# Kernel tuning notes

Hardware: AMD Instinct MI355X
Metric: run time of the kernel (lower is better)

## Reference

```python
import jax, jax.numpy as jnp
import numpy as np
import math

B, S, D = 2, 2048, 512
H = 8
DEPTH = D // H
MAX_REL = 1024
NEG_INF = -1.0e9


def skew(t):
    # t: (..., r, c). Pad a zero column on the left, reshape to move relative
    # logits into their absolute positions (Music Transformer skew trick).
    r, c = t.shape[-2], t.shape[-1]
    padded = jnp.pad(t, [(0, 0)] * (t.ndim - 1) + [(1, 0)])
    s = padded.reshape(-1, c + 1, r)[:, 1:]
    return s.reshape(t.shape)


def setup_inputs() -> dict:
    key = jax.random.key(0)
    ks = jax.random.split(key, 12)
    sc = 1.0 / math.sqrt(D)
    return {
        "q": jax.random.normal(ks[0], (B, S, D), jnp.float32),
        "k": jax.random.normal(ks[1], (B, S, D), jnp.float32),
        "v": jax.random.normal(ks[2], (B, S, D), jnp.float32),
        "mask": jax.random.randint(ks[3], (B, 1, S, S), 0, 2, jnp.int32),
        "Wq_w": jax.random.normal(ks[4], (D, D), jnp.float32) * sc,
        "Wq_b": jnp.zeros((D,), jnp.float32),
        "Wk_w": jax.random.normal(ks[5], (D, D), jnp.float32) * sc,
        "Wk_b": jnp.zeros((D,), jnp.float32),
        "Wv_w": jax.random.normal(ks[6], (D, D), jnp.float32) * sc,
        "Wv_b": jnp.zeros((D,), jnp.float32),
        "E": jax.random.normal(ks[7], (MAX_REL, D), jnp.float32),
        "Wo_w": jax.random.normal(ks[8], (D, D), jnp.float32) * sc,
        "Wo_b": jnp.zeros((D,), jnp.float32),
    }


def reference(q, k, v, mask, Wq_w, Wq_b, Wk_w, Wk_b, Wv_w, Wv_b, E, Wo_w, Wo_b):
    # Linear projections (torch Linear: x @ W^T + b)
    qp = q @ Wq_w.T + Wq_b
    kp = k @ Wk_w.T + Wk_b
    vp = v @ Wv_w.T + Wv_b

    # Required relative position embeddings for seq_len S (S >= MAX_REL here:
    # repeat E[0] for the first S-MAX_REL positions, then the full table).
    n_rep = max(0, S - MAX_REL)
    e = jnp.concatenate([jnp.tile(E[0:1], (n_rep, 1)), E[max(0, MAX_REL - S):]], axis=0)  # (S, D)

    # Split heads: (B,S,D)->(B,H,S,depth); e: (S,D)->(H,S,depth)
    qh = qp.reshape(B, S, H, DEPTH).transpose(0, 2, 1, 3)
    kh = kp.reshape(B, S, H, DEPTH).transpose(0, 2, 1, 3)
    vh = vp.reshape(B, S, H, DEPTH).transpose(0, 2, 1, 3)
    eh = e.reshape(S, H, DEPTH).transpose(1, 0, 2)

    QKt = jnp.einsum('bhqd,bhkd->bhqk', qh, kh)
    Srel = skew(jnp.einsum('bhqd,hkd->bhqk', qh, eh))
    logits = (QKt + Srel) / math.sqrt(DEPTH)
    logits = logits + mask.astype(logits.dtype) * NEG_INF
    attn = jnp.einsum('bhqk,bhkd->bhqd', jax.nn.softmax(logits, axis=-1), vh)

    # Merge heads and output projection
    out = attn.transpose(0, 2, 1, 3).reshape(B, S, D)
    return out @ Wo_w.T + Wo_b
```

## Files before the change

### kernel.cpp

```cpp
#include <hip/hip_runtime.h>
#include <hip/hip_bf16.h>

#define BB 2
#define SS 2048
#define DD 512
#define HH 8
#define DP 64
#define MR 1024

typedef __attribute__((ext_vector_type(8))) short bf16x8;
typedef __attribute__((ext_vector_type(4))) float floatx4;

static __device__ __forceinline__ unsigned short f2b(float x) {
    __hip_bfloat16 h = __float2bfloat16(x);
    return *reinterpret_cast<unsigned short*>(&h);
}
static __device__ __forceinline__ float b2f(unsigned short u) {
    __hip_bfloat16 h = *reinterpret_cast<__hip_bfloat16*>(&u);
    return __bfloat162float(h);
}
static __device__ __forceinline__ void gll16(const void* g, void* l) {
    __builtin_amdgcn_global_load_lds(
        (const __attribute__((address_space(1))) void*)g,
        (__attribute__((address_space(3))) void*)l, 16, 0, 0);
}
static __device__ __forceinline__ int xoff(int ks, int quad, int row) {
    return (((ks * 4 + quad) ^ (row & 7)) * 16);
}

__global__ __launch_bounds__(256) void prep_kernel(
    const float* __restrict__ Wq, const float* __restrict__ Wk,
    const float* __restrict__ Wv, const float* __restrict__ Wo,
    const float* __restrict__ E,  const float* __restrict__ q,
    const float* __restrict__ k,  const float* __restrict__ v,
    const int* __restrict__ mask,
    unsigned short* __restrict__ Wqb, unsigned short* __restrict__ Wkb,
    unsigned short* __restrict__ Wvb, unsigned short* __restrict__ Wob,
    unsigned short* __restrict__ Eb,  unsigned short* __restrict__ qb16,
    unsigned short* __restrict__ kb16, unsigned short* __restrict__ vb16,
    unsigned long long* __restrict__ bits)
{
    const int blk = blockIdx.x;
    if (blk < 7680) {
        const int gid = blk * 256 + threadIdx.x;
        const float* src; unsigned short* dst; int off;
        if      (gid < 65536)   { src = Wq; dst = Wqb;  off = gid; }
        else if (gid < 131072)  { src = Wk; dst = Wkb;  off = gid - 65536; }
        else if (gid < 196608)  { src = Wv; dst = Wvb;  off = gid - 131072; }
        else if (gid < 262144)  { src = Wo; dst = Wob;  off = gid - 196608; }
        else if (gid < 393216)  { src = E;  dst = Eb;   off = gid - 262144; }
        else if (gid < 917504)  { src = q;  dst = qb16; off = gid - 393216; }
        else if (gid < 1441792) { src = k;  dst = kb16; off = gid - 917504; }
        else                    { src = v;  dst = vb16; off = gid - 1441792; }
        float4 x = ((const float4*)src)[off];
        ushort4 u; u.x = f2b(x.x); u.y = f2b(x.y); u.z = f2b(x.z); u.w = f2b(x.w);
        ((ushort4*)dst)[off] = u;
    } else {
        const size_t wid = (size_t)(blk - 7680) * 4 + (threadIdx.x >> 6);
        const int lane = threadIdx.x & 63;
        const int mv = mask[wid * 64 + lane];
        unsigned long long bal = __ballot(mv != 0);
        if (lane == 0) bits[wid] = bal;
    }
}

__global__ __launch_bounds__(256) void gemm_proj(
    const unsigned short* __restrict__ Xq, const unsigned short* __restrict__ Xk,
    const unsigned short* __restrict__ Xv,
    const unsigned short* __restrict__ Wqb, const unsigned short* __restrict__ Wkb,
    const unsigned short* __restrict__ Wvb,
    const float* __restrict__ bq, const float* __restrict__ bk,
    const float* __restrict__ bv,
    unsigned short* __restrict__ qp, unsigned short* __restrict__ kp,
    unsigned short* __restrict__ vpT)
{
    const int z = blockIdx.z;
    const unsigned short* A  = (z == 0) ? Xq : (z == 1) ? Xk : Xv;
    const unsigned short* Wb = (z == 0) ? Wqb : (z == 1) ? Wkb : Wvb;
    const float* bias        = (z == 0) ? bq : (z == 1) ? bk : bv;

    __shared__ __align__(16) char parena[16384];
    char* AsB = parena;
    char* WsB = parena + 8192;
    const int t = threadIdx.x, lane = t & 63, w = t >> 6;
    const int quad = lane >> 4, l15 = lane & 15;
    const int wm = w >> 1, wn = w & 1;
    const int m0 = blockIdx.x * 64, n0 = blockIdx.y * 64;

    int wrow[2], wcol[2];
#pragma unroll
    for (int i = 0; i < 2; i++) {
        const int c = w * 128 + i * 64 + lane;
        wrow[i] = c >> 3; wcol[i] = (c & 7) ^ (wrow[i] & 7);
    }

    floatx4 acc[2][2];
#pragma unroll
    for (int i = 0; i < 2; i++)
#pragma unroll
        for (int j = 0; j < 2; j++) acc[i][j] = (floatx4){0.f, 0.f, 0.f, 0.f};

    for (int k0 = 0; k0 < 512; k0 += 64) {
        if (k0) __syncthreads();
#pragma unroll
        for (int i = 0; i < 2; i++) {
            gll16(A  + (size_t)(m0 + wrow[i]) * 512 + k0 + wcol[i] * 8,
                  AsB + (w * 2 + i) * 1024);
            gll16(Wb + (size_t)(n0 + wrow[i]) * 512 + k0 + wcol[i] * 8,
                  WsB + (w * 2 + i) * 1024);
        }
        __syncthreads();
#pragma unroll
        for (int ks = 0; ks < 2; ks++) {
            bf16x8 a0 = *(const bf16x8*)(AsB + (wm * 32 + l15) * 128 + xoff(ks, quad, l15));
            bf16x8 a1 = *(const bf16x8*)(AsB + (wm * 32 + 16 + l15) * 128 + xoff(ks, quad, l15));
            bf16x8 b0 = *(const bf16x8*)(WsB + (wn * 32 + l15) * 128 + xoff(ks, quad, l15));
            bf16x8 b1 = *(const bf16x8*)(WsB + (wn * 32 + 16 + l15) * 128 + xoff(ks, quad, l15));
            acc[0][0] = __builtin_amdgcn_mfma_f32_16x16x32_bf16(a0, b0, acc[0][0], 0, 0, 0);
            acc[0][1] = __builtin_amdgcn_mfma_f32_16x16x32_bf16(a0, b1, acc[0][1], 0, 0, 0);
            acc[1][0] = __builtin_amdgcn_mfma_f32_16x16x32_bf16(a1, b0, acc[1][0], 0, 0, 0);
            acc[1][1] = __builtin_amdgcn_mfma_f32_16x16x32_bf16(a1, b1, acc[1][1], 0, 0, 0);
        }
    }

    if (z < 2) {
        unsigned short* Out = (z == 0) ? qp : kp;
#pragma unroll
        for (int sub = 0; sub < 2; sub++)
#pragma unroll
            for (int ct = 0; ct < 2; ct++) {
                const int n = n0 + wn * 32 + ct * 16 + l15;
                const float bvl = bias[n];
#pragma unroll
                for (int r = 0; r < 4; r++) {
                    const size_t m = (size_t)(m0 + wm * 32 + sub * 16 + quad * 4 + r);
                    Out[m * 512 + n] = f2b(acc[sub][ct][r] + bvl);
                }
            }
    } else {
        __syncthreads();
        unsigned short* Ls = (unsigned short*)parena;
#pragma unroll
        for (int sub = 0; sub < 2; sub++)
#pragma unroll
            for (int ct = 0; ct < 2; ct++) {
                const int dcol = wn * 32 + ct * 16 + l15;
                const float bvl = bias[n0 + dcol];
#pragma unroll
                for (int r = 0; r < 4; r++) {
                    const int scol = wm * 32 + sub * 16 + quad * 4 + r;
                    Ls[dcol * 72 + scol] = f2b(acc[sub][ct][r] + bvl);
                }
            }
        __syncthreads();
        const int bb = blockIdx.x >> 5, s0 = (blockIdx.x & 31) * 64, hh = blockIdx.y;
#pragma unroll
        for (int p = 0; p < 2; p++) {
            const int idx = p * 256 + t;
            const int row = idx >> 3, c8 = (idx & 7) * 8;
            *(uint4*)&vpT[((size_t)(bb * 8 + hh) * 64 + row) * SS + s0 + c8] =
                *(const uint4*)&Ls[row * 72 + c8];
        }
    }
}

__global__ __launch_bounds__(256) void gemm_out(
    const unsigned short* __restrict__ A, const unsigned short* __restrict__ Wb,
    const float* __restrict__ bias, float* __restrict__ Out)
{
    __shared__ __align__(16) char parena[16384];
    char* AsB = parena;
    char* WsB = parena + 8192;
    const int t = threadIdx.x, lane = t & 63, w = t >> 6;
    const int quad = lane >> 4, l15 = lane & 15;
    const int wm = w >> 1, wn = w & 1;
    const int m0 = blockIdx.x * 64, n0 = blockIdx.y * 64;

    int wrow[2], wcol[2];
#pragma unroll
    for (int i = 0; i < 2; i++) {
        const int c = w * 128 + i * 64 + lane;
        wrow[i] = c >> 3; wcol[i] = (c & 7) ^ (wrow[i] & 7);
    }

    floatx4 acc[2][2];
#pragma unroll
    for (int i = 0; i < 2; i++)
#pragma unroll
        for (int j = 0; j < 2; j++) acc[i][j] = (floatx4){0.f, 0.f, 0.f, 0.f};

    for (int k0 = 0; k0 < 512; k0 += 64) {
        if (k0) __syncthreads();
#pragma unroll
        for (int i = 0; i < 2; i++) {
            gll16(A  + (size_t)(m0 + wrow[i]) * 512 + k0 + wcol[i] * 8,
                  AsB + (w * 2 + i) * 1024);
            gll16(Wb + (size_t)(n0 + wrow[i]) * 512 + k0 + wcol[i] * 8,
                  WsB + (w * 2 + i) * 1024);
        }
        __syncthreads();
#pragma unroll
        for (int ks = 0; ks < 2; ks++) {
            bf16x8 a0 = *(const bf16x8*)(AsB + (wm * 32 + l15) * 128 + xoff(ks, quad, l15));
            bf16x8 a1 = *(const bf16x8*)(AsB + (wm * 32 + 16 + l15) * 128 + xoff(ks, quad, l15));
            bf16x8 b0 = *(const bf16x8*)(WsB + (wn * 32 + l15) * 128 + xoff(ks, quad, l15));
            bf16x8 b1 = *(const bf16x8*)(WsB + (wn * 32 + 16 + l15) * 128 + xoff(ks, quad, l15));
            acc[0][0] = __builtin_amdgcn_mfma_f32_16x16x32_bf16(a0, b0, acc[0][0], 0, 0, 0);
            acc[0][1] = __builtin_amdgcn_mfma_f32_16x16x32_bf16(a0, b1, acc[0][1], 0, 0, 0);
            acc[1][0] = __builtin_amdgcn_mfma_f32_16x16x32_bf16(a1, b0, acc[1][0], 0, 0, 0);
            acc[1][1] = __builtin_amdgcn_mfma_f32_16x16x32_bf16(a1, b1, acc[1][1], 0, 0, 0);
        }
    }
#pragma unroll
    for (int sub = 0; sub < 2; sub++)
#pragma unroll
        for (int ct = 0; ct < 2; ct++) {
            const int n = n0 + wn * 32 + ct * 16 + l15;
            const float bvl = bias[n];
#pragma unroll
            for (int r = 0; r < 4; r++) {
                const size_t m = (size_t)(m0 + wm * 32 + sub * 16 + quad * 4 + r);
                Out[m * 512 + n] = acc[sub][ct][r] + bvl;
            }
        }
}

__global__ __launch_bounds__(256) void relg_kernel(
    const unsigned short* __restrict__ qp, const unsigned short* __restrict__ Eb,
    unsigned short* __restrict__ G)
{
    __shared__ unsigned short Ls[64 * 72];
    const int t = threadIdx.x, lane = t & 63, w = t >> 6;
    const int quad = lane >> 4, l15 = lane & 15;
    const int bh = blockIdx.z, b = bh >> 3, h = bh & 7;
    const int i0b = blockIdx.x * 64, t0 = blockIdx.y * 64;

    const unsigned short* Ar = qp + ((size_t)b * SS + i0b + w * 16 + l15) * DD + h * DP;
    bf16x8 a0 = *(const bf16x8*)(Ar + quad * 8);
    bf16x8 a1 = *(const bf16x8*)(Ar + 32 + quad * 8);

    floatx4 acc[4];
#pragma unroll
    for (int ct = 0; ct < 4; ct++) acc[ct] = (floatx4){0.f, 0.f, 0.f, 0.f};
#pragma unroll
    for (int ct = 0; ct < 4; ct++) {
        const unsigned short* Br = Eb + (size_t)(t0 + ct * 16 + l15) * DD + h * DP;
        bf16x8 b0 = *(const bf16x8*)(Br + quad * 8);
        bf16x8 b1 = *(const bf16x8*)(Br + 32 + quad * 8);
        acc[ct] = __builtin_amdgcn_mfma_f32_16x16x32_bf16(a0, b0, acc[ct], 0, 0, 0);
        acc[ct] = __builtin_amdgcn_mfma_f32_16x16x32_bf16(a1, b1, acc[ct], 0, 0, 0);
    }
#pragma unroll
    for (int ct = 0; ct < 4; ct++)
#pragma unroll
        for (int r = 0; r < 4; r++)
            Ls[(w * 16 + quad * 4 + r) * 72 + ct * 16 + l15] = f2b(acc[ct][r]);
    __syncthreads();
#pragma unroll
    for (int p = 0; p < 2; p++) {
        const int idx = p * 256 + t;
        const int row = idx >> 3, c8 = (idx & 7) * 8;
        *(uint4*)&G[((size_t)bh * SS + i0b + row) * MR + t0 + c8] =
            *(const uint4*)&Ls[row * 72 + c8];
    }
}

__global__ __launch_bounds__(256, 4) void attn_kernel(
    const unsigned short* __restrict__ qp, const unsigned short* __restrict__ kp,
    const unsigned short* __restrict__ vpT, const unsigned long long* __restrict__ mb64,
    const unsigned short* __restrict__ G, unsigned short* __restrict__ ao)
{
    __shared__ __align__(16) char smem[33024];
    char* KsB = smem;
    char* VtB = smem + 16384;

    const int t = threadIdx.x, lane = t & 63, w = t >> 6;
    const int quad = lane >> 4, l15 = lane & 15;
    const int wr = w >> 1, kh = w & 1;
    const int bh = blockIdx.y, b = bh >> 3, h = bh & 7;
    const int i0w = blockIdx.x * 32 + wr * 16;
    const int gi = i0w + l15;

    const unsigned short* kb = kp + (size_t)b * SS * DD + h * DP;
    const unsigned short* vb = vpT + (size_t)bh * DP * SS;
    const unsigned short* Gb = G + (size_t)bh * SS * MR;
    const unsigned long long* mrow64 = mb64 + ((size_t)b * SS + gi) * 32;

    const unsigned short* qrow = qp + ((size_t)b * SS + gi) * DD + h * DP;
    bf16x8 qf0 = *(const bf16x8*)(qrow + quad * 8);
    bf16x8 qf1 = *(const bf16x8*)(qrow + 32 + quad * 8);

    const unsigned short* pdiag = Gb + (size_t)gi * 1023;
    const float d0a = b2f(Gb[(size_t)gi * MR]);
    const float d0b = b2f(Gb[(size_t)min(gi + 1, SS - 1) * MR]);

    char* KhB = KsB + kh * 8192;
    char* VhB = VtB + kh * 8192;
    char* PtB = KhB + wr * 4096;

    int koff[4], voff[4];
#pragma unroll
    for (int i = 0; i < 4; i++) {
        const int c = wr * 256 + i * 64 + lane;
        const int crow = c >> 3, ccol = (c & 7) ^ (crow & 7);
        koff[i] = crow * DD + ccol * 8;
        voff[i] = crow * SS + ccol * 8;
    }

    floatx4 oacc[4];
#pragma unroll
    for (int ct = 0; ct < 4; ct++) oacc[ct] = (floatx4){0.f, 0.f, 0.f, 0.f};
    float lsum = 0.0f;

    for (int it = 0; it < 16; it++) {
        const int k0 = (kh * 16 + it) * 64;
        __syncthreads();
#pragma unroll
        for (int i = 0; i < 4; i++)
            gll16(kb + (size_t)k0 * DD + koff[i], KhB + (wr * 4 + i) * 1024);
#pragma unroll
        for (int i = 0; i < 4; i++)
            gll16(vb + k0 + voff[i], VhB + (wr * 4 + i) * 1024);

        const unsigned long long mwv = mrow64[kh * 16 + it];
        const unsigned int mlo = (unsigned int)mwv;
        const unsigned int mhi = (unsigned int)(mwv >> 32);

        float relv[4][4];
#pragma unroll
        for (int ct = 0; ct < 4; ct++) {
            const int k0c = k0 + ct * 16;
            const int gj0 = k0c + quad * 4;
            const int dmax = i0w + 15 - k0c;
            const int dmin = i0w - (k0c + 15);
            if (dmin >= MR) {
#pragma unroll
                for (int r = 0; r < 4; r++) relv[ct][r] = d0a;
            } else if (dmin >= 0 && dmax <= MR - 1) {
#pragma unroll
                for (int r = 0; r < 4; r++) relv[ct][r] = b2f(pdiag[1023 + gj0 + r]);
            } else if (dmax <= -2 && dmin >= -(MR + 1)) {
#pragma unroll
                for (int r = 0; r < 4; r++) relv[ct][r] = d0b;
            } else if (dmax <= -(MR + 2)) {
#pragma unroll
                for (int r = 0; r < 4; r++) relv[ct][r] = b2f(pdiag[gj0 - 2 + r]);
            } else {
#pragma unroll
                for (int r = 0; r < 4; r++) {
                    const int gj = gj0 + r;
                    const int dd = gi - gj;
                    float rl;
                    if (dd >= MR) rl = d0a;
                    else if (dd >= 0) rl = b2f(pdiag[1023 + gj]);
                    else if (dd == -1) rl = 0.0f;
                    else if (dd >= -(MR + 1)) rl = d0b;
                    else rl = b2f(pdiag[gj - 2]);
                    relv[ct][r] = rl;
                }
            }
        }
        __syncthreads();

        ushort4 pu[4];
#pragma unroll
        for (int ct = 0; ct < 4; ct++) {
            const unsigned int half = (ct < 2) ? mlo : mhi;
            const unsigned int nib = (half >> ((ct & 1) * 16 + quad * 4)) & 0xFu;
            floatx4 acc;
#pragma unroll
            for (int r = 0; r < 4; r++)
                acc[r] = relv[ct][r] + (((nib >> r) & 1u) ? -8.0e9f : 0.0f);
            const int row = ct * 16 + l15;
            bf16x8 kf0 = *(const bf16x8*)(KhB + row * 128 + xoff(0, quad, l15));
            bf16x8 kf1 = *(const bf16x8*)(KhB + row * 128 + xoff(1, quad, l15));
            acc = __builtin_amdgcn_mfma_f32_16x16x32_bf16(kf0, qf0, acc, 0, 0, 0);
            acc = __builtin_amdgcn_mfma_f32_16x16x32_bf16(kf1, qf1, acc, 0, 0, 0);
            const float p0 = __expf(acc[0] * 0.125f - 18.75f);
            const float p1 = __expf(acc[1] * 0.125f - 18.75f);
            const float p2 = __expf(acc[2] * 0.125f - 18.75f);
            const float p3 = __expf(acc[3] * 0.125f - 18.75f);
            lsum += (p0 + p1) + (p2 + p3);
            pu[ct].x = f2b(p0); pu[ct].y = f2b(p1);
            pu[ct].z = f2b(p2); pu[ct].w = f2b(p3);
        }
        __syncthreads();

#pragma unroll
        for (int ct = 0; ct < 4; ct++)
            *(ushort4*)(PtB + l15 * 144 + ct * 32 + quad * 8) = pu[ct];

        bf16x8 pt0 = *(const bf16x8*)(PtB + l15 * 144 + quad * 16);
        bf16x8 pt1 = *(const bf16x8*)(PtB + l15 * 144 + 64 + quad * 16);
#pragma unroll
        for (int ct = 0; ct < 4; ct++) {
            const int drow = ct * 16 + l15;
            bf16x8 vf0 = *(const bf16x8*)(VhB + drow * 128 + xoff(0, quad, l15));
            bf16x8 vf1 = *(const bf16x8*)(VhB + drow * 128 + xoff(1, quad, l15));
            oacc[ct] = __builtin_amdgcn_mfma_f32_16x16x32_bf16(vf0, pt0, oacc[ct], 0, 0, 0);
            oacc[ct] = __builtin_amdgcn_mfma_f32_16x16x32_bf16(vf1, pt1, oacc[ct], 0, 0, 0);
        }
    }

    lsum += __shfl_xor(lsum, 16);
    lsum += __shfl_xor(lsum, 32);

    __syncthreads();
    float* OmW = (float*)(VtB + wr * 4352);
    float* MlW = (float*)(smem + 32768);
    if (kh == 1) {
#pragma unroll
        for (int ct = 0; ct < 4; ct++)
            *(floatx4*)&OmW[l15 * 68 + ct * 16 + quad * 4] = oacc[ct];
        if (lane < 16) MlW[wr * 16 + lane] = lsum;
    }
    __syncthreads();
    if (kh == 0) {
        const float inv = 1.0f / (lsum + MlW[wr * 16 + l15]);
#pragma unroll
        for (int ct = 0; ct < 4; ct++) {
            floatx4 o1 = *(const floatx4*)&OmW[l15 * 68 + ct * 16 + quad * 4];
            ushort4 u;
            u.x = f2b((oacc[ct][0] + o1[0]) * inv);
            u.y = f2b((oacc[ct][1] + o1[1]) * inv);
            u.z = f2b((oacc[ct][2] + o1[2]) * inv);
            u.w = f2b((oacc[ct][3] + o1[3]) * inv);
            *(ushort4*)&ao[((size_t)b * SS + gi) * DD + h * DP + ct * 16 + quad * 4] = u;
        }
    }
}

extern "C" void kernel_launch(void* const* d_in, const int* in_sizes, int n_in,
                              void* d_out, int out_size, void* d_ws, size_t ws_size,
                              hipStream_t stream)
{
    const float* q    = (const float*)d_in[0];
    const float* k    = (const float*)d_in[1];
    const float* v    = (const float*)d_in[2];
    const int*   mask = (const int*)d_in[3];
    const float* Wq_w = (const float*)d_in[4];
    const float* Wq_b = (const float*)d_in[5];
    const float* Wk_w = (const float*)d_in[6];
    const float* Wk_b = (const float*)d_in[7];
    const float* Wv_w = (const float*)d_in[8];
    const float* Wv_b = (const float*)d_in[9];
    const float* E    = (const float*)d_in[10];
    const float* Wo_w = (const float*)d_in[11];
    const float* Wo_b = (const float*)d_in[12];
    float* out = (float*)d_out;

    char* ws = (char*)d_ws;
    unsigned short* G    = (unsigned short*)ws;
    unsigned short* qp   = (unsigned short*)(ws + 67108864);
    unsigned short* kp   = qp + 2097152;
    unsigned short* vpT  = kp + 2 * 2097152;
    unsigned short* qb16 = vpT + 2097152;
    unsigned short* kb16 = qb16 + 2097152;
    unsigned short* vb16 = kb16 + 2097152;
    unsigned short* aob  = qb16;
    unsigned long long* mbits = (unsigned long long*)(ws + 67108864 + 7 * 4194304);
    unsigned short* Wqb = (unsigned short*)(ws + 67108864 + 7 * 4194304 + 1048576);
    unsigned short* Wkb = Wqb + 262144;
    unsigned short* Wvb = Wkb + 262144;
    unsigned short* Wob = Wvb + 262144;
    unsigned short* Ebf = Wob + 262144;

    dim3 blk(256);
    hipLaunchKernelGGL(prep_kernel, dim3(40448), blk, 0, stream,
                       Wq_w, Wk_w, Wv_w, Wo_w, E, q, k, v, mask,
                       Wqb, Wkb, Wvb, Wob, Ebf, qb16, kb16, vb16, mbits);
    hipLaunchKernelGGL(gemm_proj, dim3(64, 8, 3), blk, 0, stream,
                       qb16, kb16, vb16, Wqb, Wkb, Wvb, Wq_b, Wk_b, Wv_b,
                       qp, kp, vpT);
    hipLaunchKernelGGL(relg_kernel, dim3(32, 16, 16), blk, 0, stream, qp, Ebf, G);
    hipLaunchKernelGGL(attn_kernel, dim3(64, 16), blk, 0, stream,
                       qp, kp, vpT, mbits, G, aob);
    hipLaunchKernelGGL(gemm_out, dim3(64, 8), blk, 0, stream, aob, Wob, Wo_b, out);
}
```

Measured before the change: 266.1 us.

## Double-buffer attention K/V tiles with prefetch, halve GEMM M-tiles

The attention kernel now processes 32-key tiles and double-buffers K and V in shared memory. The next tile's global-to-LDS loads are issued before computing the current one, and the mask word and relative-position values for the next tile are loaded early, which removes one barrier per iteration. The projection and output GEMMs use 32-row M tiles, doubling the grid for more parallelism at the cost of less reuse per block. It also adds smaller MFMA chunks per iteration and more loop iterations.

```diff
diff --git a/kernel.cpp b/kernel.cpp
--- a/kernel.cpp
+++ b/kernel.cpp
@@ -79,88 +79,76 @@
     const unsigned short* Wb = (z == 0) ? Wqb : (z == 1) ? Wkb : Wvb;
     const float* bias        = (z == 0) ? bq : (z == 1) ? bk : bv;
 
-    __shared__ __align__(16) char parena[16384];
+    __shared__ __align__(16) char parena[12288];
     char* AsB = parena;
-    char* WsB = parena + 8192;
+    char* WsB = parena + 4096;
     const int t = threadIdx.x, lane = t & 63, w = t >> 6;
     const int quad = lane >> 4, l15 = lane & 15;
     const int wm = w >> 1, wn = w & 1;
-    const int m0 = blockIdx.x * 64, n0 = blockIdx.y * 64;
-
+    const int m0 = blockIdx.x * 32, n0 = blockIdx.y * 64;
+
+    const int pa = w * 64 + lane;
+    const int arow = pa >> 3, acol = (pa & 7) ^ (arow & 7);
     int wrow[2], wcol[2];
 #pragma unroll
     for (int i = 0; i < 2; i++) {
-        const int c = w * 128 + i * 64 + lane;
-        wrow[i] = c >> 3; wcol[i] = (c & 7) ^ (wrow[i] & 7);
-    }
-
-    floatx4 acc[2][2];
-#pragma unroll
-    for (int i = 0; i < 2; i++)
-#pragma unroll
-        for (int j = 0; j < 2; j++) acc[i][j] = (floatx4){0.f, 0.f, 0.f, 0.f};
+        const int c = w * 2 + i;
+        const int p = c * 64 + lane;
+        wrow[i] = p >> 3; wcol[i] = (p & 7) ^ (wrow[i] & 7);
+    }
+
+    floatx4 acc[2];
+    acc[0] = (floatx4){0.f, 0.f, 0.f, 0.f};
+    acc[1] = (floatx4){0.f, 0.f, 0.f, 0.f};
 
     for (int k0 = 0; k0 < 512; k0 += 64) {
         if (k0) __syncthreads();
-#pragma unroll
-        for (int i = 0; i < 2; i++) {
-            gll16(A  + (size_t)(m0 + wrow[i]) * 512 + k0 + wcol[i] * 8,
-                  AsB + (w * 2 + i) * 1024);
+        gll16(A + (size_t)(m0 + arow) * 512 + k0 + acol * 8, AsB + w * 1024);
+#pragma unroll
+        for (int i = 0; i < 2; i++)
             gll16(Wb + (size_t)(n0 + wrow[i]) * 512 + k0 + wcol[i] * 8,
                   WsB + (w * 2 + i) * 1024);
-        }
         __syncthreads();
 #pragma unroll
         for (int ks = 0; ks < 2; ks++) {
-            bf16x8 a0 = *(const bf16x8*)(AsB + (wm * 32 + l15) * 128 + xoff(ks, quad, l15));
-            bf16x8 a1 = *(const bf16x8*)(AsB + (wm * 32 + 16 + l15) * 128 + xoff(ks, quad, l15));
+            bf16x8 a0 = *(const bf16x8*)(AsB + (wm * 16 + l15) * 128 + xoff(ks, quad, l15));
             bf16x8 b0 = *(const bf16x8*)(WsB + (wn * 32 + l15) * 128 + xoff(ks, quad, l15));
             bf16x8 b1 = *(const bf16x8*)(WsB + (wn * 32 + 16 + l15) * 128 + xoff(ks, quad, l15));
-            acc[0][0] = __builtin_amdgcn_mfma_f32_16x16x32_bf16(a0, b0, acc[0][0], 0, 0, 0);
-            acc[0][1] = __builtin_amdgcn_mfma_f32_16x16x32_bf16(a0, b1, acc[0][1], 0, 0, 0);
-            acc[1][0] = __builtin_amdgcn_mfma_f32_16x16x32_bf16(a1, b0, acc[1][0], 0, 0, 0);
-            acc[1][1] = __builtin_amdgcn_mfma_f32_16x16x32_bf16(a1, b1, acc[1][1], 0, 0, 0);
+            acc[0] = __builtin_amdgcn_mfma_f32_16x16x32_bf16(a0, b0, acc[0], 0, 0, 0);
+            acc[1] = __builtin_amdgcn_mfma_f32_16x16x32_bf16(a0, b1, acc[1], 0, 0, 0);
         }
     }
 
     if (z < 2) {
         unsigned short* Out = (z == 0) ? qp : kp;
 #pragma unroll
-        for (int sub = 0; sub < 2; sub++)
-#pragma unroll
-            for (int ct = 0; ct < 2; ct++) {
-                const int n = n0 + wn * 32 + ct * 16 + l15;
-                const float bvl = bias[n];
-#pragma unroll
-                for (int r = 0; r < 4; r++) {
-                    const size_t m = (size_t)(m0 + wm * 32 + sub * 16 + quad * 4 + r);
-                    Out[m * 512 + n] = f2b(acc[sub][ct][r] + bvl);
-                }
+        for (int ct = 0; ct < 2; ct++) {
+            const int n = n0 + wn * 32 + ct * 16 + l15;
+            const float bvl = bias[n];
+#pragma unroll
+            for (int r = 0; r < 4; r++) {
+                const size_t m = (size_t)(m0 + wm * 16 + quad * 4 + r);
+                Out[m * 512 + n] = f2b(acc[ct][r] + bvl);
             }
+        }
     } else {
         __syncthreads();
         unsigned short* Ls = (unsigned short*)parena;
 #pragma unroll
-        for (int sub = 0; sub < 2; sub++)
-#pragma unroll
-            for (int ct = 0; ct < 2; ct++) {
-                const int dcol = wn * 32 + ct * 16 + l15;
-                const float bvl = bias[n0 + dcol];
-#pragma unroll
-                for (int r = 0; r < 4; r++) {
-                    const int scol = wm * 32 + sub * 16 + quad * 4 + r;
-                    Ls[dcol * 72 + scol] = f2b(acc[sub][ct][r] + bvl);
-                }
+        for (int ct = 0; ct < 2; ct++) {
+            const int dcol = wn * 32 + ct * 16 + l15;
+            const float bvl = bias[n0 + dcol];
+#pragma unroll
+            for (int r = 0; r < 4; r++) {
+                const int srow = wm * 16 + quad * 4 + r;
+                Ls[dcol * 40 + srow] = f2b(acc[ct][r] + bvl);
             }
+        }
         __syncthreads();
-        const int bb = blockIdx.x >> 5, s0 = (blockIdx.x & 31) * 64, hh = blockIdx.y;
-#pragma unroll
-        for (int p = 0; p < 2; p++) {
-            const int idx = p * 256 + t;
-            const int row = idx >> 3, c8 = (idx & 7) * 8;
-            *(uint4*)&vpT[((size_t)(bb * 8 + hh) * 64 + row) * SS + s0 + c8] =
-                *(const uint4*)&Ls[row * 72 + c8];
-        }
+        const int bb = blockIdx.x >> 6, s0 = (blockIdx.x & 63) * 32, hh = blockIdx.y;
+        const int drow = t >> 2, sc8 = (t & 3) * 8;
+        *(uint4*)&vpT[((size_t)(bb * 8 + hh) * 64 + drow) * SS + s0 + sc8] =
+            *(const uint4*)&Ls[drow * 40 + sc8];
     }
 }
 
@@ -168,61 +156,55 @@
     const unsigned short* __restrict__ A, const unsigned short* __restrict__ Wb,
     const float* __restrict__ bias, float* __restrict__ Out)
 {
-    __shared__ __align__(16) char parena[16384];
+    __shared__ __align__(16) char parena[12288];
     char* AsB = parena;
-    char* WsB = parena + 8192;
+    char* WsB = parena + 4096;
     const int t = threadIdx.x, lane = t & 63, w = t >> 6;
     const int quad = lane >> 4, l15 = lane & 15;
     const int wm = w >> 1, wn = w & 1;
-    const int m0 = blockIdx.x * 64, n0 = blockIdx.y * 64;
-
+    const int m0 = blockIdx.x * 32, n0 = blockIdx.y * 64;
+
+    const int pa = w * 64 + lane;
+    const int arow = pa >> 3, acol = (pa & 7) ^ (arow & 7);
     int wrow[2], wcol[2];
 #pragma unroll
     for (int i = 0; i < 2; i++) {
-        const int c = w * 128 + i * 64 + lane;
-        wrow[i] = c >> 3; wcol[i] = (c & 7) ^ (wrow[i] & 7);
-    }
-
-    floatx4 acc[2][2];
-#pragma unroll
-    for (int i = 0; i < 2; i++)
-#pragma unroll
-        for (int j = 0; j < 2; j++) acc[i][j] = (floatx4){0.f, 0.f, 0.f, 0.f};
+        const int c = w * 2 + i;
+        const int p = c * 64 + lane;
+        wrow[i] = p >> 3; wcol[i] = (p & 7) ^ (wrow[i] & 7);
+    }
+
+    floatx4 acc[2];
+    acc[0] = (floatx4){0.f, 0.f, 0.f, 0.f};
+    acc[1] = (floatx4){0.f, 0.f, 0.f, 0.f};
 
     for (int k0 = 0; k0 < 512; k0 += 64) {
         if (k0) __syncthreads();
-#pragma unroll
-        for (int i = 0; i < 2; i++) {
-            gll16(A  + (size_t)(m0 + wrow[i]) * 512 + k0 + wcol[i] * 8,
-                  AsB + (w * 2 + i) * 1024);
+        gll16(A + (size_t)(m0 + arow) * 512 + k0 + acol * 8, AsB + w * 1024);
+#pragma unroll
+        for (int i = 0; i < 2; i++)
             gll16(Wb + (size_t)(n0 + wrow[i]) * 512 + k0 + wcol[i] * 8,
                   WsB + (w * 2 + i) * 1024);
-        }
         __syncthreads();
 #pragma unroll
         for (int ks = 0; ks < 2; ks++) {
-            bf16x8 a0 = *(const bf16x8*)(AsB + (wm * 32 + l15) * 128 + xoff(ks, quad, l15));
-            bf16x8 a1 = *(const bf16x8*)(AsB + (wm * 32 + 16 + l15) * 128 + xoff(ks, quad, l15));
+            bf16x8 a0 = *(const bf16x8*)(AsB + (wm * 16 + l15) * 128 + xoff(ks, quad, l15));
             bf16x8 b0 = *(const bf16x8*)(WsB + (wn * 32 + l15) * 128 + xoff(ks, quad, l15));
             bf16x8 b1 = *(const bf16x8*)(WsB + (wn * 32 + 16 + l15) * 128 + xoff(ks, quad, l15));
-            acc[0][0] = __builtin_amdgcn_mfma_f32_16x16x32_bf16(a0, b0, acc[0][0], 0, 0, 0);
-            acc[0][1] = __builtin_amdgcn_mfma_f32_16x16x32_bf16(a0, b1, acc[0][1], 0, 0, 0);
-            acc[1][0] = __builtin_amdgcn_mfma_f32_16x16x32_bf16(a1, b0, acc[1][0], 0, 0, 0);
-            acc[1][1] = __builtin_amdgcn_mfma_f32_16x16x32_bf16(a1, b1, acc[1][1], 0, 0, 0);
-        }
-    }
-#pragma unroll
-    for (int sub = 0; sub < 2; sub++)
-#pragma unroll
-        for (int ct = 0; ct < 2; ct++) {
-            const int n = n0 + wn * 32 + ct * 16 + l15;
-            const float bvl = bias[n];
-#pragma unroll
-            for (int r = 0; r < 4; r++) {
-                const size_t m = (size_t)(m0 + wm * 32 + sub * 16 + quad * 4 + r);
-                Out[m * 512 + n] = acc[sub][ct][r] + bvl;
-            }
-        }
+            acc[0] = __builtin_amdgcn_mfma_f32_16x16x32_bf16(a0, b0, acc[0], 0, 0, 0);
+            acc[1] = __builtin_amdgcn_mfma_f32_16x16x32_bf16(a0, b1, acc[1], 0, 0, 0);
+        }
+    }
+#pragma unroll
+    for (int ct = 0; ct < 2; ct++) {
+        const int n = n0 + wn * 32 + ct * 16 + l15;
+        const float bvl = bias[n];
+#pragma unroll
+        for (int r = 0; r < 4; r++) {
+            const size_t m = (size_t)(m0 + wm * 16 + quad * 4 + r);
+            Out[m * 512 + n] = acc[ct][r] + bvl;
+        }
+    }
 }
 
 __global__ __launch_bounds__(256) void relg_kernel(
@@ -265,15 +247,51 @@
     }
 }
 
+static __device__ __forceinline__ void load_rel(
+    const unsigned short* __restrict__ pdiag, int i0w, int gi, int k0,
+    float d0a, float d0b, int quad, float relv[2][4])
+{
+#pragma unroll
+    for (int ct = 0; ct < 2; ct++) {
+        const int k0c = k0 + ct * 16;
+        const int gj0 = k0c + quad * 4;
+        const int dmax = i0w + 15 - k0c;
+        const int dmin = i0w - (k0c + 15);
+        if (dmin >= MR) {
+#pragma unroll
+            for (int r = 0; r < 4; r++) relv[ct][r] = d0a;
+        } else if (dmin >= 0 && dmax <= MR - 1) {
+#pragma unroll
+            for (int r = 0; r < 4; r++) relv[ct][r] = b2f(pdiag[1023 + gj0 + r]);
+        } else if (dmax <= -2 && dmin >= -(MR + 1)) {
+#pragma unroll
+            for (int r = 0; r < 4; r++) relv[ct][r] = d0b;
+        } else if (dmax <= -(MR + 2)) {
+#pragma unroll
+            for (int r = 0; r < 4; r++) relv[ct][r] = b2f(pdiag[gj0 - 2 + r]);
+        } else {
+#pragma unroll
+            for (int r = 0; r < 4; r++) {
+                const int gj = gj0 + r;
+                const int dd = gi - gj;
+                float rl;
+                if (dd >= MR) rl = d0a;
+                else if (dd >= 0) rl = b2f(pdiag[1023 + gj]);
+                else if (dd == -1) rl = 0.0f;
+                else if (dd >= -(MR + 1)) rl = d0b;
+                else rl = b2f(pdiag[gj - 2]);
+                relv[ct][r] = rl;
+            }
+        }
+    }
+}
+
 __global__ __launch_bounds__(256, 4) void attn_kernel(
     const unsigned short* __restrict__ qp, const unsigned short* __restrict__ kp,
-    const unsigned short* __restrict__ vpT, const unsigned long long* __restrict__ mb64,
+    const unsigned short* __restrict__ vpT, const unsigned int* __restrict__ mb32,
     const unsigned short* __restrict__ G, unsigned short* __restrict__ ao)
 {
-    __shared__ __align__(16) char smem[33024];
-    char* KsB = smem;
-    char* VtB = smem + 16384;
-
+    __shared__ __align__(16) char smem[38016];
     const int t = threadIdx.x, lane = t & 63, w = t >> 6;
     const int quad = lane >> 4, l15 = lane & 15;
     const int wr = w >> 1, kh = w & 1;
@@ -284,7 +302,7 @@
     const unsigned short* kb = kp + (size_t)b * SS * DD + h * DP;
     const unsigned short* vb = vpT + (size_t)bh * DP * SS;
     const unsigned short* Gb = G + (size_t)bh * SS * MR;
-    const unsigned long long* mrow64 = mb64 + ((size_t)b * SS + gi) * 32;
+    const unsigned int* mrow32 = mb32 + ((size_t)b * SS + gi) * 64;
 
     const unsigned short* qrow = qp + ((size_t)b * SS + gi) * DD + h * DP;
     bf16x8 qf0 = *(const bf16x8*)(qrow + quad * 8);
@@ -294,17 +312,20 @@
     const float d0a = b2f(Gb[(size_t)gi * MR]);
     const float d0b = b2f(Gb[(size_t)min(gi + 1, SS - 1) * MR]);
 
-    char* KhB = KsB + kh * 8192;
-    char* VhB = VtB + kh * 8192;
-    char* PtB = KhB + wr * 4096;
-
-    int koff[4], voff[4];
-#pragma unroll
-    for (int i = 0; i < 4; i++) {
-        const int c = wr * 256 + i * 64 + lane;
-        const int crow = c >> 3, ccol = (c & 7) ^ (crow & 7);
-        koff[i] = crow * DD + ccol * 8;
-        voff[i] = crow * SS + ccol * 8;
+    char* Kh = smem + kh * 8192;
+    char* Vh = smem + 16384 + kh * 8192;
+    char* Pt = smem + 32768 + w * 1280;
+
+    int kofs[2], vofs[2], dst[2];
+#pragma unroll
+    for (int i = 0; i < 2; i++) {
+        const int c = wr * 2 + i;
+        const int p = c * 64 + lane;
+        const int krow = p >> 3, kcol = (p & 7) ^ (krow & 7);
+        kofs[i] = krow * DD + kcol * 8;
+        const int vrow = p >> 2, vcol = (p & 3) ^ (vrow & 3);
+        vofs[i] = vrow * SS + vcol * 8;
+        dst[i] = c * 1024;
     }
 
     floatx4 oacc[4];
@@ -312,93 +333,78 @@
     for (int ct = 0; ct < 4; ct++) oacc[ct] = (floatx4){0.f, 0.f, 0.f, 0.f};
     float lsum = 0.0f;
 
-    for (int it = 0; it < 16; it++) {
-        const int k0 = (kh * 16 + it) * 64;
+    {
+        const int k0 = kh * 1024;
+        gll16(kb + (size_t)k0 * DD + kofs[0], Kh + dst[0]);
+        gll16(kb + (size_t)k0 * DD + kofs[1], Kh + dst[1]);
+        gll16(vb + k0 + vofs[0], Vh + dst[0]);
+        gll16(vb + k0 + vofs[1], Vh + dst[1]);
+    }
+    unsigned int mwv = mrow32[kh * 32];
+    float relv[2][4];
+    load_rel(pdiag, i0w, gi, kh * 1024, d0a, d0b, quad, relv);
+
+    for (int it = 0; it < 32; it++) {
+        const int cur = it & 1;
         __syncthreads();
-#pragma unroll
-        for (int i = 0; i < 4; i++)
-            gll16(kb + (size_t)k0 * DD + koff[i], KhB + (wr * 4 + i) * 1024);
-#pragma unroll
-        for (int i = 0; i < 4; i++)
-            gll16(vb + k0 + voff[i], VhB + (wr * 4 + i) * 1024);
-
-        const unsigned long long mwv = mrow64[kh * 16 + it];
-        const unsigned int mlo = (unsigned int)mwv;
-        const unsigned int mhi = (unsigned int)(mwv >> 32);
-
-        float relv[4][4];
-#pragma unroll
-        for (int ct = 0; ct < 4; ct++) {
-            const int k0c = k0 + ct * 16;
-            const int gj0 = k0c + quad * 4;
-            const int dmax = i0w + 15 - k0c;
-            const int dmin = i0w - (k0c + 15);
-            if (dmin >= MR) {
-#pragma unroll
-                for (int r = 0; r < 4; r++) relv[ct][r] = d0a;
-            } else if (dmin >= 0 && dmax <= MR - 1) {
-#pragma unroll
-                for (int r = 0; r < 4; r++) relv[ct][r] = b2f(pdiag[1023 + gj0 + r]);
-            } else if (dmax <= -2 && dmin >= -(MR + 1)) {
-#pragma unroll
-                for (int r = 0; r < 4; r++) relv[ct][r] = d0b;
-            } else if (dmax <= -(MR + 2)) {
-#pragma unroll
-                for (int r = 0; r < 4; r++) relv[ct][r] = b2f(pdiag[gj0 - 2 + r]);
-            } else {
-#pragma unroll
-                for (int r = 0; r < 4; r++) {
-                    const int gj = gj0 + r;
-                    const int dd = gi - gj;
-                    float rl;
-                    if (dd >= MR) rl = d0a;
-                    else if (dd >= 0) rl = b2f(pdiag[1023 + gj]);
-                    else if (dd == -1) rl = 0.0f;
-                    else if (dd >= -(MR + 1)) rl = d0b;
-                    else rl = b2f(pdiag[gj - 2]);
-                    relv[ct][r] = rl;
-                }
-            }
-        }
-        __syncthreads();
-
-        ushort4 pu[4];
-#pragma unroll
-        for (int ct = 0; ct < 4; ct++) {
-            const unsigned int half = (ct < 2) ? mlo : mhi;
-            const unsigned int nib = (half >> ((ct & 1) * 16 + quad * 4)) & 0xFu;
-            floatx4 acc;
+        if (it + 1 < 32) {
+            const int k0n = kh * 1024 + (it + 1) * 32;
+            const int nb = (cur ^ 1) * 4096;
+            gll16(kb + (size_t)k0n * DD + kofs[0], Kh + nb + dst[0]);
+            gll16(kb + (size_t)k0n * DD + kofs[1], Kh + nb + dst[1]);
+            gll16(vb + k0n + vofs[0], Vh + nb + dst[0]);
+            gll16(vb + k0n + vofs[1], Vh + nb + dst[1]);
+        }
+        const unsigned int mcur = mwv;
+        float relc[2][4];
+#pragma unroll
+        for (int ct = 0; ct < 2; ct++)
+#pragma unroll
+            for (int r = 0; r < 4; r++) relc[ct][r] = relv[ct][r];
+
+        char* Kc = Kh + cur * 4096;
+        char* Vc = Vh + cur * 4096;
+
+        floatx4 acc[2];
+#pragma unroll
+        for (int ct = 0; ct < 2; ct++) {
+            const unsigned int nib = (mcur >> (ct * 16 + quad * 4)) & 0xFu;
+            floatx4 a;
 #pragma unroll
             for (int r = 0; r < 4; r++)
-                acc[r] = relv[ct][r] + (((nib >> r) & 1u) ? -8.0e9f : 0.0f);
+                a[r] = relc[ct][r] + (((nib >> r) & 1u) ? -8.0e9f : 0.0f);
             const int row = ct * 16 + l15;
-            bf16x8 kf0 = *(const bf16x8*)(KhB + row * 128 + xoff(0, quad, l15));
-            bf16x8 kf1 = *(const bf16x8*)(KhB + row * 128 + xoff(1, quad, l15));
-            acc = __builtin_amdgcn_mfma_f32_16x16x32_bf16(kf0, qf0, acc, 0, 0, 0);
-            acc = __builtin_amdgcn_mfma_f32_16x16x32_bf16(kf1, qf1, acc, 0, 0, 0);
-            const float p0 = __expf(acc[0] * 0.125f - 18.75f);
-            const float p1 = __expf(acc[1] * 0.125f - 18.75f);
-            const float p2 = __expf(acc[2] * 0.125f - 18.75f);
-            const float p3 = __expf(acc[3] * 0.125f - 18.75f);
+            bf16x8 kf0 = *(const bf16x8*)(Kc + row * 128 + ((quad ^ (l15 & 7)) * 16));
+            bf16x8 kf1 = *(const bf16x8*)(Kc + row * 128 + (((4 + quad) ^ (l15 & 7)) * 16));
+            a = __builtin_amdgcn_mfma_f32_16x16x32_bf16(kf0, qf0, a, 0, 0, 0);
+            a = __builtin_amdgcn_mfma_f32_16x16x32_bf16(kf1, qf1, a, 0, 0, 0);
+            acc[ct] = a;
+        }
+
+        {
+            const int itn = (it + 1 < 32) ? it + 1 : 31;
+            mwv = mrow32[kh * 32 + itn];
+            load_rel(pdiag, i0w, gi, kh * 1024 + itn * 32, d0a, d0b, quad, relv);
+        }
+
+#pragma unroll
+        for (int ct = 0; ct < 2; ct++) {
+            const float p0 = __expf(acc[ct][0] * 0.125f - 18.75f);
+            const float p1 = __expf(acc[ct][1] * 0.125f - 18.75f);
+            const float p2 = __expf(acc[ct][2] * 0.125f - 18.75f);
+            const float p3 = __expf(acc[ct][3] * 0.125f - 18.75f);
             lsum += (p0 + p1) + (p2 + p3);
-            pu[ct].x = f2b(p0); pu[ct].y = f2b(p1);
-            pu[ct].z = f2b(p2); pu[ct].w = f2b(p3);
-        }
-        __syncthreads();
-
-#pragma unroll
-        for (int ct = 0; ct < 4; ct++)
-            *(ushort4*)(PtB + l15 * 144 + ct * 32 + quad * 8) = pu[ct];
-
-        bf16x8 pt0 = *(const bf16x8*)(PtB + l15 * 144 + quad * 16);
-        bf16x8 pt1 = *(const bf16x8*)(PtB + l15 * 144 + 64 + quad * 16);
+            ushort4 u;
+            u.x = f2b(p0); u.y = f2b(p1); u.z = f2b(p2); u.w = f2b(p3);
+            *(ushort4*)(Pt + l15 * 80 + ct * 32 + quad * 8) = u;
+        }
+
+        bf16x8 pt = *(const bf16x8*)(Pt + l15 * 80 + quad * 16);
 #pragma unroll
         for (int ct = 0; ct < 4; ct++) {
             const int drow = ct * 16 + l15;
-            bf16x8 vf0 = *(const bf16x8*)(VhB + drow * 128 + xoff(0, quad, l15));
-            bf16x8 vf1 = *(const bf16x8*)(VhB + drow * 128 + xoff(1, quad, l15));
-            oacc[ct] = __builtin_amdgcn_mfma_f32_16x16x32_bf16(vf0, pt0, oacc[ct], 0, 0, 0);
-            oacc[ct] = __builtin_amdgcn_mfma_f32_16x16x32_bf16(vf1, pt1, oacc[ct], 0, 0, 0);
+            bf16x8 vf = *(const bf16x8*)(Vc + drow * 64 + ((quad ^ (drow & 3)) * 16));
+            oacc[ct] = __builtin_amdgcn_mfma_f32_16x16x32_bf16(vf, pt, oacc[ct], 0, 0, 0);
         }
     }
 
@@ -406,8 +412,8 @@
     lsum += __shfl_xor(lsum, 32);
 
     __syncthreads();
-    float* OmW = (float*)(VtB + wr * 4352);
-    float* MlW = (float*)(smem + 32768);
+    float* OmW = (float*)(smem + wr * 4352);
+    float* MlW = (float*)(smem + 37888);
     if (kh == 1) {
 #pragma unroll
         for (int ct = 0; ct < 4; ct++)
@@ -469,11 +475,11 @@
     hipLaunchKernelGGL(prep_kernel, dim3(40448), blk, 0, stream,
                        Wq_w, Wk_w, Wv_w, Wo_w, E, q, k, v, mask,
                        Wqb, Wkb, Wvb, Wob, Ebf, qb16, kb16, vb16, mbits);
-    hipLaunchKernelGGL(gemm_proj, dim3(64, 8, 3), blk, 0, stream,
+    hipLaunchKernelGGL(gemm_proj, dim3(128, 8, 3), blk, 0, stream,
                        qb16, kb16, vb16, Wqb, Wkb, Wvb, Wq_b, Wk_b, Wv_b,
                        qp, kp, vpT);
     hipLaunchKernelGGL(relg_kernel, dim3(32, 16, 16), blk, 0, stream, qp, Ebf, G);
     hipLaunchKernelGGL(attn_kernel, dim3(64, 16), blk, 0, stream,
-                       qp, kp, vpT, mbits, G, aob);
-    hipLaunchKernelGGL(gemm_out, dim3(64, 8), blk, 0, stream, aob, Wob, Wo_b, out);
-}
+                       qp, kp, vpT, (const unsigned int*)mbits, G, aob);
+    hipLaunchKernelGGL(gemm_out, dim3(128, 8), blk, 0, stream, aob, Wob, Wo_b, out);
+}
```

Measured after the change: 254.7 us. -4.3%, faster.
